# Optimization experiments

Measured on AMD Instinct MI355X. Metric: run time of the kernel, lower is better.

## Reference

```python
import jax, jax.numpy as jnp
import numpy as np

N = 4194304   # number of query coordinates
D = 8         # feature width of xs
V = 1048576   # number of active sparse entries (param table size)


def setup_inputs() -> dict:
    key = jax.random.key(0)
    k1, k2, k3 = jax.random.split(key, 3)
    xs = jax.random.normal(k1, (N, D), dtype=jnp.float32)
    idx = jax.random.randint(k2, (N,), 0, V, dtype=jnp.int64)
    params = jax.random.normal(k3, (V, 1), dtype=jnp.float32)  # one scalar param per sparse entry
    return {"xs": xs, "idx": idx, "params": params}


def reference(xs, idx, params):
    # Original torch loop: out[i] = params[idx[i]] * xs[i]; fused gather-multiply.
    return params[idx] * xs  # [N,1] broadcast against [N,D] -> [N,D]
```

## Files before the change

kernel.cpp:

```cpp
#include <hip/hip_runtime.h>
#include <hip/hip_bf16.h>


__global__ __launch_bounds__(256) void spvar_kernel(
    const float4* __restrict__ xs4,
    const int*    __restrict__ idx,
    const float*  __restrict__ params,
    float4*       __restrict__ out4,
    int n4)
{
    int tid = blockIdx.x * blockDim.x + threadIdx.x;
    if (tid >= n4) return;
    int row = tid >> 1;
    float p = params[idx[row]];
    float4 x = xs4[tid];
    float4 o;
    o.x = x.x * p;
    o.y = x.y * p;
    o.z = x.z * p;
    o.w = x.w * p;
    out4[tid] = o;
}

extern "C" void kernel_launch(void* const* d_in, const int* in_sizes, int n_in,
                              void* d_out, int out_size, void* d_ws, size_t ws_size,
                              hipStream_t stream) {
    const float* xs     = (const float*)d_in[0];
    const int*   idx    = (const int*)d_in[1];
    const float* params = (const float*)d_in[2];

    const int n4 = out_size / 4;
    const int block = 256;
    const int grid = (n4 + block - 1) / block;

    spvar_kernel<<<grid, block, 0, stream>>>(
        (const float4*)xs, idx, params, (float4*)d_out, n4);
}
```

Measured before the change: 253.4 us.

## Process four rows per thread with nontemporal loads and stores

Each thread now handles one full row (two float4 halves) for four rows spaced a grid-stride apart, batching the index and param gathers before the streaming loads. Streaming xs loads and output stores use nontemporal hints, so single-use data should not evict the params table from cache. Coalescing changes because each thread reads 32 contiguous bytes instead of adjacent threads reading adjacent 16-byte halves, and the grid becomes a quarter as large, which may reduce occupancy and latency hiding.

```diff
diff --git a/kernel.cpp b/kernel.cpp
--- a/kernel.cpp
+++ b/kernel.cpp
@@ -1,25 +1,68 @@
 #include <hip/hip_runtime.h>
-#include <hip/hip_bf16.h>
 
 
+typedef float f32x4 __attribute__((ext_vector_type(4)));
+
 __global__ __launch_bounds__(256) void spvar_kernel(
-    const float4* __restrict__ xs4,
-    const int*    __restrict__ idx,
-    const float*  __restrict__ params,
-    float4*       __restrict__ out4,
-    int n4)
+    const f32x4* __restrict__ xs4,
+    const int*   __restrict__ idx,
+    const float* __restrict__ params,
+    f32x4*       __restrict__ out4,
+    int nrows, int stride)
 {
-    int tid = blockIdx.x * blockDim.x + threadIdx.x;
-    if (tid >= n4) return;
-    int row = tid >> 1;
-    float p = params[idx[row]];
-    float4 x = xs4[tid];
-    float4 o;
-    o.x = x.x * p;
-    o.y = x.y * p;
-    o.z = x.z * p;
-    o.w = x.w * p;
-    out4[tid] = o;
+    const int t = blockIdx.x * blockDim.x + threadIdx.x;
+    const int r0 = t;
+    const int r1 = t + stride;
+    const int r2 = t + 2 * stride;
+    const int r3 = t + 3 * stride;
+
+    if (r3 < nrows) {
+        const int i0 = __builtin_nontemporal_load(idx + r0);
+        const int i1 = __builtin_nontemporal_load(idx + r1);
+        const int i2 = __builtin_nontemporal_load(idx + r2);
+        const int i3 = __builtin_nontemporal_load(idx + r3);
+
+        const float p0 = params[i0];
+        const float p1 = params[i1];
+        const float p2 = params[i2];
+        const float p3 = params[i3];
+
+        f32x4 a0 = __builtin_nontemporal_load(xs4 + 2 * r0);
+        f32x4 b0 = __builtin_nontemporal_load(xs4 + 2 * r0 + 1);
+        f32x4 a1 = __builtin_nontemporal_load(xs4 + 2 * r1);
+        f32x4 b1 = __builtin_nontemporal_load(xs4 + 2 * r1 + 1);
+        f32x4 a2 = __builtin_nontemporal_load(xs4 + 2 * r2);
+        f32x4 b2 = __builtin_nontemporal_load(xs4 + 2 * r2 + 1);
+        f32x4 a3 = __builtin_nontemporal_load(xs4 + 2 * r3);
+        f32x4 b3 = __builtin_nontemporal_load(xs4 + 2 * r3 + 1);
+
+        a0 *= p0; b0 *= p0;
+        a1 *= p1; b1 *= p1;
+        a2 *= p2; b2 *= p2;
+        a3 *= p3; b3 *= p3;
+
+        __builtin_nontemporal_store(a0, out4 + 2 * r0);
+        __builtin_nontemporal_store(b0, out4 + 2 * r0 + 1);
+        __builtin_nontemporal_store(a1, out4 + 2 * r1);
+        __builtin_nontemporal_store(b1, out4 + 2 * r1 + 1);
+        __builtin_nontemporal_store(a2, out4 + 2 * r2);
+        __builtin_nontemporal_store(b2, out4 + 2 * r2 + 1);
+        __builtin_nontemporal_store(a3, out4 + 2 * r3);
+        __builtin_nontemporal_store(b3, out4 + 2 * r3 + 1);
+    } else {
+        #pragma unroll
+        for (int u = 0; u < 4; ++u) {
+            const int r = t + u * stride;
+            if (r < nrows) {
+                const float p = params[idx[r]];
+                f32x4 a = __builtin_nontemporal_load(xs4 + 2 * r);
+                f32x4 b = __builtin_nontemporal_load(xs4 + 2 * r + 1);
+                a *= p; b *= p;
+                __builtin_nontemporal_store(a, out4 + 2 * r);
+                __builtin_nontemporal_store(b, out4 + 2 * r + 1);
+            }
+        }
+    }
 }
 
 extern "C" void kernel_launch(void* const* d_in, const int* in_sizes, int n_in,
@@ -29,10 +72,12 @@
     const int*   idx    = (const int*)d_in[1];
     const float* params = (const float*)d_in[2];
 
-    const int n4 = out_size / 4;
+    const int nrows = out_size / 8;
     const int block = 256;
-    const int grid = (n4 + block - 1) / block;
+    const int rows_per_thread = 4;
+    const int grid = (nrows + block * rows_per_thread - 1) / (block * rows_per_thread);
+    const int stride = grid * block;
 
     spvar_kernel<<<grid, block, 0, stream>>>(
-        (const float4*)xs, idx, params, (float4*)d_out, n4);
+        (const f32x4*)xs, idx, params, (f32x4*)d_out, nrows, stride);
 }
```

Measured after the change: 266.1 us. 5.0% more time.

## Split gather into separate kernel writing workspace, then stream scale per row

Applied to the files above, without the earlier changes.

Replaces the fused per-float4 kernel with two passes: one kernel gathers params[idx] for four rows per thread into a workspace buffer, and a second streams xs and multiplies each 8-wide row by its gathered scalar. The goal is to separate the random-access gather from the bandwidth-bound streaming so each phase has better memory-level parallelism, and to stop reading idx and params twice per row. In exchange it adds a second launch and an extra write and read of the gathered values. A fused one-row-per-thread kernel is used as a fallback when the workspace is too small.

```diff
diff --git a/kernel.cpp b/kernel.cpp
--- a/kernel.cpp
+++ b/kernel.cpp
@@ -1,25 +1,67 @@
 #include <hip/hip_runtime.h>
-#include <hip/hip_bf16.h>
 
 
-__global__ __launch_bounds__(256) void spvar_kernel(
-    const float4* __restrict__ xs4,
-    const int*    __restrict__ idx,
-    const float*  __restrict__ params,
-    float4*       __restrict__ out4,
-    int n4)
+typedef float f32x4 __attribute__((ext_vector_type(4)));
+typedef int   i32x4 __attribute__((ext_vector_type(4)));
+
+__global__ __launch_bounds__(256) void spvar_gather(
+    const int*   __restrict__ idx,
+    const float* __restrict__ params,
+    float*       __restrict__ pvals,
+    int nrows)
 {
-    int tid = blockIdx.x * blockDim.x + threadIdx.x;
-    if (tid >= n4) return;
-    int row = tid >> 1;
-    float p = params[idx[row]];
-    float4 x = xs4[tid];
-    float4 o;
-    o.x = x.x * p;
-    o.y = x.y * p;
-    o.z = x.z * p;
-    o.w = x.w * p;
-    out4[tid] = o;
+    const int t = blockIdx.x * blockDim.x + threadIdx.x;
+    const int r = t * 4;
+    if (r + 3 < nrows) {
+        const i32x4 i4 = *(const i32x4*)(idx + r);
+        f32x4 p;
+        p.x = params[i4.x];
+        p.y = params[i4.y];
+        p.z = params[i4.z];
+        p.w = params[i4.w];
+        *(f32x4*)(pvals + r) = p;
+    } else {
+        #pragma unroll
+        for (int u = 0; u < 4; ++u)
+            if (r + u < nrows) pvals[r + u] = params[idx[r + u]];
+    }
+}
+
+__global__ __launch_bounds__(256) void spvar_scale(
+    const f32x4* __restrict__ xs4,
+    const float* __restrict__ pvals,
+    f32x4*       __restrict__ out4,
+    int nrows)
+{
+    const int t = blockIdx.x * blockDim.x + threadIdx.x;
+    if (t < nrows) {
+        const float p = pvals[t];
+        f32x4 a = xs4[2 * t];
+        f32x4 b = xs4[2 * t + 1];
+        a *= p;
+        b *= p;
+        out4[2 * t]     = a;
+        out4[2 * t + 1] = b;
+    }
+}
+
+__global__ __launch_bounds__(256) void spvar_fused(
+    const f32x4* __restrict__ xs4,
+    const int*   __restrict__ idx,
+    const float* __restrict__ params,
+    f32x4*       __restrict__ out4,
+    int nrows)
+{
+    const int t = blockIdx.x * blockDim.x + threadIdx.x;
+    if (t < nrows) {
+        const float p = params[idx[t]];
+        f32x4 a = xs4[2 * t];
+        f32x4 b = xs4[2 * t + 1];
+        a *= p;
+        b *= p;
+        out4[2 * t]     = a;
+        out4[2 * t + 1] = b;
+    }
 }
 
 extern "C" void kernel_launch(void* const* d_in, const int* in_sizes, int n_in,
@@ -29,10 +71,21 @@
     const int*   idx    = (const int*)d_in[1];
     const float* params = (const float*)d_in[2];
 
-    const int n4 = out_size / 4;
+    const int nrows = out_size / 8;
     const int block = 256;
-    const int grid = (n4 + block - 1) / block;
 
-    spvar_kernel<<<grid, block, 0, stream>>>(
-        (const float4*)xs, idx, params, (float4*)d_out, n4);
+    if (ws_size >= (size_t)nrows * sizeof(float)) {
+        float* pvals = (float*)d_ws;
+
+        const int grid1 = (nrows / 4 + block - 1) / block;
+        spvar_gather<<<grid1, block, 0, stream>>>(idx, params, pvals, nrows);
+
+        const int grid2 = (nrows + block - 1) / block;
+        spvar_scale<<<grid2, block, 0, stream>>>(
+            (const f32x4*)xs, pvals, (f32x4*)d_out, nrows);
+    } else {
+        const int grid = (nrows + block - 1) / block;
+        spvar_fused<<<grid, block, 0, stream>>>(
+            (const f32x4*)xs, idx, params, (f32x4*)d_out, nrows);
+    }
 }
```

After: 268.2 us. +5.9%, slower.
